# Kernel tuning notes

Measured on AMD Instinct MI355X. Metric: run time of the kernel, lower is better.

The kernel has to match this reference:

```python
import jax, jax.numpy as jnp
import numpy as np

N, K, D, M = 100000, 16, 128, 3  # nodes, edges-per-node (degree), feat dim, max cardinality


def setup_inputs() -> dict:
    key = jax.random.key(0)
    k1, k2 = jax.random.split(key)
    x = jax.random.normal(k1, (N, D), dtype=jnp.float32)
    nbr = jax.random.randint(k2, (N, K), 0, N)  # edge {v, nbr[v,k]} for each incident hyperedge
    return {"x": x, "nbr": nbr}


def reference(x, nbr):
    # Hyperedge cardinality c=2, max cardinality M=3.
    # adj_coef: alpha = C(2,0)*2^3 - C(2,1)*1^3 = 6 ; a = c/alpha = 1/3 ; divided by degree K.
    coef = jnp.float32((2.0 / 6.0) / K)
    xu = x[nbr]  # [N, K, D] gathered neighbor features (irregular access)
    # For edge {v,u}: valid size-3 combinations-with-replacement containing both nodes are
    # [u,u,v] (multiplicity 2 after removing v) and [u,v,v] (multiplicity 1):
    #   2 * x_v * x_u + x_u * x_u
    out = coef * jnp.sum(2.0 * x[:, None, :] * xu + xu * xu, axis=1)  # [N, D]
    return out
```

## Files before the change

kernel.cpp:

```cpp
#include <hip/hip_runtime.h>

#define N_NODES 100000
#define K_DEG   16
#define D_FEAT  128

__global__ __launch_bounds__(256) void convert_bf16_kernel(
    const float* __restrict__ x, unsigned int* __restrict__ xb2 )
{
    int gid = blockIdx.x * blockDim.x + threadIdx.x;
    const float4* x4 = (const float4*)x;
    float4 f = x4[gid];
    unsigned int u0 = __float_as_uint(f.x), u1 = __float_as_uint(f.y);
    unsigned int u2 = __float_as_uint(f.z), u3 = __float_as_uint(f.w);
    unsigned int h0 = (u0 + 0x7fffu + ((u0 >> 16) & 1u)) >> 16;
    unsigned int h1 = (u1 + 0x7fffu + ((u1 >> 16) & 1u)) >> 16;
    unsigned int h2 = (u2 + 0x7fffu + ((u2 >> 16) & 1u)) >> 16;
    unsigned int h3 = (u3 + 0x7fffu + ((u3 >> 16) & 1u)) >> 16;
    uint2 o; o.x = h0 | (h1 << 16); o.y = h2 | (h3 << 16);
    ((uint2*)xb2)[gid] = o;
}

__device__ __forceinline__ void unpack2(unsigned int p, float& a, float& b) {
    a = __uint_as_float(p << 16);
    b = __uint_as_float(p & 0xffff0000u);
}

__global__ __launch_bounds__(256, 4) void TMessagePassing_kernel(
    const unsigned int* __restrict__ xb,
    const int*          __restrict__ nbr,
    float*              __restrict__ out)
{
    int gid = blockIdx.x * blockDim.x + threadIdx.x;
    int v   = gid >> 5;
    int col = gid & 31;

    const uint2* __restrict__ xb2 = (const uint2*)xb;

    const int4* __restrict__ nb4 = (const int4*)(nbr + (size_t)v * K_DEG);
    int4 n0 = nb4[0];
    int4 n1 = nb4[1];
    int4 n2 = nb4[2];
    int4 n3 = nb4[3];
    int idx[K_DEG] = { n0.x, n0.y, n0.z, n0.w,
                       n1.x, n1.y, n1.z, n1.w,
                       n2.x, n2.y, n2.z, n2.w,
                       n3.x, n3.y, n3.z, n3.w };

    uint2 xvp = xb2[(size_t)v * 32 + col];

    uint2 xu[K_DEG];
#pragma unroll
    for (int k = 0; k < K_DEG; ++k) {
        xu[k] = xb2[(size_t)idx[k] * 32 + col];
    }
    __builtin_amdgcn_sched_barrier(0);

    float s1a = 0.f, s1b = 0.f, s1c = 0.f, s1d = 0.f;
    float s2a = 0.f, s2b = 0.f, s2c = 0.f, s2d = 0.f;
#pragma unroll
    for (int k = 0; k < K_DEG; ++k) {
        float a, b, c, d;
        unpack2(xu[k].x, a, b);
        unpack2(xu[k].y, c, d);
        s1a += a; s1b += b; s1c += c; s1d += d;
        s2a += a * a; s2b += b * b; s2c += c * c; s2d += d * d;
    }

    float va, vb, vc, vd;
    unpack2(xvp.x, va, vb);
    unpack2(xvp.y, vc, vd);

    const float coef = 1.0f / 48.0f;
    float4 o;
    o.x = coef * (2.f * va * s1a + s2a);
    o.y = coef * (2.f * vb * s1b + s2b);
    o.z = coef * (2.f * vc * s1c + s2c);
    o.w = coef * (2.f * vd * s1d + s2d);

    ((float4*)out)[(size_t)v * 32 + col] = o;
}

__global__ __launch_bounds__(256, 4) void TMessagePassing_fp32_kernel(
    const float* __restrict__ x, const int* __restrict__ nbr, float* __restrict__ out)
{
    int gid = blockIdx.x * blockDim.x + threadIdx.x;
    int v = gid >> 5, col = gid & 31;
    const float4* x4 = (const float4*)x;
    const int4* nb4 = (const int4*)(nbr + (size_t)v * K_DEG);
    int4 n0 = nb4[0], n1 = nb4[1], n2 = nb4[2], n3 = nb4[3];
    int idx[K_DEG] = { n0.x, n0.y, n0.z, n0.w, n1.x, n1.y, n1.z, n1.w,
                       n2.x, n2.y, n2.z, n2.w, n3.x, n3.y, n3.z, n3.w };
    float4 xv = x4[(size_t)v * 32 + col];
    float4 s1 = make_float4(0, 0, 0, 0), s2 = make_float4(0, 0, 0, 0);
#pragma unroll
    for (int k = 0; k < K_DEG; ++k) {
        float4 u = x4[(size_t)idx[k] * 32 + col];
        s1.x += u.x; s1.y += u.y; s1.z += u.z; s1.w += u.w;
        s2.x += u.x * u.x; s2.y += u.y * u.y; s2.z += u.z * u.z; s2.w += u.w * u.w;
    }
    const float coef = 1.0f / 48.0f;
    float4 o;
    o.x = coef * (2.f * xv.x * s1.x + s2.x);
    o.y = coef * (2.f * xv.y * s1.y + s2.y);
    o.z = coef * (2.f * xv.z * s1.z + s2.z);
    o.w = coef * (2.f * xv.w * s1.w + s2.w);
    ((float4*)out)[(size_t)v * 32 + col] = o;
}

extern "C" void kernel_launch(void* const* d_in, const int* in_sizes, int n_in,
                              void* d_out, int out_size, void* d_ws, size_t ws_size,
                              hipStream_t stream) {
    const float* x   = (const float*)d_in[0];
    const int*   nbr = (const int*)d_in[1];
    float*       out = (float*)d_out;

    const size_t need = (size_t)N_NODES * D_FEAT * 2;
    if (ws_size >= need) {
        unsigned int* xb = (unsigned int*)d_ws;
        int conv_threads = N_NODES * D_FEAT / 4;
        convert_bf16_kernel<<<conv_threads / 256, 256, 0, stream>>>(x, xb);
        int total = N_NODES * 32;
        TMessagePassing_kernel<<<total / 256 + (total % 256 != 0), 256, 0, stream>>>(xb, nbr, out);
    } else {
        int total = N_NODES * 32;
        TMessagePassing_fp32_kernel<<<total / 256 + (total % 256 != 0), 256, 0, stream>>>(x, nbr, out);
    }
}
```

Before: 153.8 us.

## Software-pipeline neighbor gathers and add nontemporal hints with higher occupancy

The monolithic 16-way gather followed by reduction is replaced with a double-buffered scheme: two groups of four gathers are in flight while the previous group is accumulated. This cuts per-thread register use, and launch bounds are raised to 8 waves per SIMD to increase occupancy. Nontemporal loads and stores are added for the neighbor indices, the bf16 conversion output and the final output, to keep streaming data from polluting cache. The trade-off is less memory-level parallelism per thread, which must be made up by the extra occupancy. There is also a risk that the nontemporal store of the bf16 table evicts data the gather kernel then reloads.

```diff
diff --git a/kernel.cpp b/kernel.cpp
--- a/kernel.cpp
+++ b/kernel.cpp
@@ -4,8 +4,12 @@
 #define K_DEG   16
 #define D_FEAT  128
 
+typedef int   v4i __attribute__((ext_vector_type(4)));
+typedef float v4f __attribute__((ext_vector_type(4)));
+typedef unsigned int v2u __attribute__((ext_vector_type(2)));
+
 __global__ __launch_bounds__(256) void convert_bf16_kernel(
-    const float* __restrict__ x, unsigned int* __restrict__ xb2 )
+    const float* __restrict__ x, unsigned int* __restrict__ xb2)
 {
     int gid = blockIdx.x * blockDim.x + threadIdx.x;
     const float4* x4 = (const float4*)x;
@@ -16,8 +20,8 @@
     unsigned int h1 = (u1 + 0x7fffu + ((u1 >> 16) & 1u)) >> 16;
     unsigned int h2 = (u2 + 0x7fffu + ((u2 >> 16) & 1u)) >> 16;
     unsigned int h3 = (u3 + 0x7fffu + ((u3 >> 16) & 1u)) >> 16;
-    uint2 o; o.x = h0 | (h1 << 16); o.y = h2 | (h3 << 16);
-    ((uint2*)xb2)[gid] = o;
+    v2u o; o.x = h0 | (h1 << 16); o.y = h2 | (h3 << 16);
+    __builtin_nontemporal_store(o, ((v2u*)xb2) + gid);
 }
 
 __device__ __forceinline__ void unpack2(unsigned int p, float& a, float& b) {
@@ -25,7 +29,21 @@
     b = __uint_as_float(p & 0xffff0000u);
 }
 
-__global__ __launch_bounds__(256, 4) void TMessagePassing_kernel(
+__device__ __forceinline__ void acc4(const uint2* g,
+    float& s1a, float& s1b, float& s1c, float& s1d,
+    float& s2a, float& s2b, float& s2c, float& s2d)
+{
+#pragma unroll
+    for (int k = 0; k < 4; ++k) {
+        float a, b, c, d;
+        unpack2(g[k].x, a, b);
+        unpack2(g[k].y, c, d);
+        s1a += a; s1b += b; s1c += c; s1d += d;
+        s2a += a * a; s2b += b * b; s2c += c * c; s2d += d * d;
+    }
+}
+
+__global__ __launch_bounds__(256, 8) void TMessagePassing_kernel(
     const unsigned int* __restrict__ xb,
     const int*          __restrict__ nbr,
     float*              __restrict__ out)
@@ -36,48 +54,54 @@
 
     const uint2* __restrict__ xb2 = (const uint2*)xb;
 
-    const int4* __restrict__ nb4 = (const int4*)(nbr + (size_t)v * K_DEG);
-    int4 n0 = nb4[0];
-    int4 n1 = nb4[1];
-    int4 n2 = nb4[2];
-    int4 n3 = nb4[3];
-    int idx[K_DEG] = { n0.x, n0.y, n0.z, n0.w,
-                       n1.x, n1.y, n1.z, n1.w,
-                       n2.x, n2.y, n2.z, n2.w,
-                       n3.x, n3.y, n3.z, n3.w };
+    const v4i* nb4 = (const v4i*)(nbr + (size_t)v * K_DEG);
+    v4i n0 = __builtin_nontemporal_load(nb4 + 0);
+    v4i n1 = __builtin_nontemporal_load(nb4 + 1);
+    v4i n2 = __builtin_nontemporal_load(nb4 + 2);
+    v4i n3 = __builtin_nontemporal_load(nb4 + 3);
 
     uint2 xvp = xb2[(size_t)v * 32 + col];
 
-    uint2 xu[K_DEG];
-#pragma unroll
-    for (int k = 0; k < K_DEG; ++k) {
-        xu[k] = xb2[(size_t)idx[k] * 32 + col];
-    }
-    __builtin_amdgcn_sched_barrier(0);
-
     float s1a = 0.f, s1b = 0.f, s1c = 0.f, s1d = 0.f;
     float s2a = 0.f, s2b = 0.f, s2c = 0.f, s2d = 0.f;
-#pragma unroll
-    for (int k = 0; k < K_DEG; ++k) {
-        float a, b, c, d;
-        unpack2(xu[k].x, a, b);
-        unpack2(xu[k].y, c, d);
-        s1a += a; s1b += b; s1c += c; s1d += d;
-        s2a += a * a; s2b += b * b; s2c += c * c; s2d += d * d;
-    }
+
+    uint2 ga[4], gb[4];
+    ga[0] = xb2[(size_t)n0.x * 32 + col];
+    ga[1] = xb2[(size_t)n0.y * 32 + col];
+    ga[2] = xb2[(size_t)n0.z * 32 + col];
+    ga[3] = xb2[(size_t)n0.w * 32 + col];
+    gb[0] = xb2[(size_t)n1.x * 32 + col];
+    gb[1] = xb2[(size_t)n1.y * 32 + col];
+    gb[2] = xb2[(size_t)n1.z * 32 + col];
+    gb[3] = xb2[(size_t)n1.w * 32 + col];
+
+    acc4(ga, s1a, s1b, s1c, s1d, s2a, s2b, s2c, s2d);
+    ga[0] = xb2[(size_t)n2.x * 32 + col];
+    ga[1] = xb2[(size_t)n2.y * 32 + col];
+    ga[2] = xb2[(size_t)n2.z * 32 + col];
+    ga[3] = xb2[(size_t)n2.w * 32 + col];
+
+    acc4(gb, s1a, s1b, s1c, s1d, s2a, s2b, s2c, s2d);
+    gb[0] = xb2[(size_t)n3.x * 32 + col];
+    gb[1] = xb2[(size_t)n3.y * 32 + col];
+    gb[2] = xb2[(size_t)n3.z * 32 + col];
+    gb[3] = xb2[(size_t)n3.w * 32 + col];
+
+    acc4(ga, s1a, s1b, s1c, s1d, s2a, s2b, s2c, s2d);
+    acc4(gb, s1a, s1b, s1c, s1d, s2a, s2b, s2c, s2d);
 
     float va, vb, vc, vd;
     unpack2(xvp.x, va, vb);
     unpack2(xvp.y, vc, vd);
 
     const float coef = 1.0f / 48.0f;
-    float4 o;
+    v4f o;
     o.x = coef * (2.f * va * s1a + s2a);
     o.y = coef * (2.f * vb * s1b + s2b);
     o.z = coef * (2.f * vc * s1c + s2c);
     o.w = coef * (2.f * vd * s1d + s2d);
 
-    ((float4*)out)[(size_t)v * 32 + col] = o;
+    __builtin_nontemporal_store(o, ((v4f*)out) + (size_t)v * 32 + col);
 }
 
 __global__ __launch_bounds__(256, 4) void TMessagePassing_fp32_kernel(
@@ -115,14 +139,13 @@
     float*       out = (float*)d_out;
 
     const size_t need = (size_t)N_NODES * D_FEAT * 2;
+    int total = N_NODES * 32;
     if (ws_size >= need) {
         unsigned int* xb = (unsigned int*)d_ws;
         int conv_threads = N_NODES * D_FEAT / 4;
         convert_bf16_kernel<<<conv_threads / 256, 256, 0, stream>>>(x, xb);
-        int total = N_NODES * 32;
         TMessagePassing_kernel<<<total / 256 + (total % 256 != 0), 256, 0, stream>>>(xb, nbr, out);
     } else {
-        int total = N_NODES * 32;
         TMessagePassing_fp32_kernel<<<total / 256 + (total % 256 != 0), 256, 0, stream>>>(x, nbr, out);
     }
 }
```

Measured after the change: 155.5 us. No clear change (+1.1%).
